# Kernel optimization log

Hardware: AMD Instinct MI355X
Metric: run time of the kernel (lower is better)

The kernel has to match this reference:

```python
import jax, jax.numpy as jnp
import numpy as np

N, IN_F, OUT_F, H = 8192, 256, 64, 4
NEG_SLOPE = 0.2


def setup_inputs() -> dict:
    key = jax.random.key(0)
    ks = jax.random.split(key, 8)
    inputs = jax.random.normal(ks[0], (N, IN_F), dtype=jnp.float32)
    # sparse-ish binary adjacency with self loops (sparse.softmax only sees nonzeros)
    adj = (jax.random.uniform(ks[1], (N, N)) < 0.05).astype(jnp.float32)
    idx = jnp.arange(N)
    adj = adj.at[idx, idx].set(1.0)
    stdv = 1.0 / np.sqrt(H * OUT_F)
    weight = jax.random.uniform(ks[2], (IN_F, H * OUT_F), minval=-stdv, maxval=stdv, dtype=jnp.float32)
    bias = jax.random.uniform(ks[3], (1, H * OUT_F), minval=-stdv, maxval=stdv, dtype=jnp.float32)
    # weight_u/v: stdv = 1/sqrt(size(-1)=1) = 1
    weight_u = jax.random.uniform(ks[4], (H, OUT_F, 1), minval=-1.0, maxval=1.0, dtype=jnp.float32)
    weight_v = jax.random.uniform(ks[5], (H, OUT_F, 1), minval=-1.0, maxval=1.0, dtype=jnp.float32)
    stdp = 1.0 / np.sqrt(IN_F)
    proj_w = jax.random.uniform(ks[6], (H * OUT_F, IN_F), minval=-stdp, maxval=stdp, dtype=jnp.float32)
    proj_b = jax.random.uniform(ks[7], (H * OUT_F,), minval=-stdp, maxval=stdp, dtype=jnp.float32)
    return {"inputs": inputs, "adj_mat": adj, "weight": weight, "weight_u": weight_u,
            "weight_v": weight_v, "bias": bias, "proj_w": proj_w, "proj_b": proj_b}


def reference(inputs, adj_mat, weight, weight_u, weight_v, bias, proj_w, proj_b):
    n = inputs.shape[0]
    support = (inputs @ weight).reshape(n, H, OUT_F).transpose(1, 0, 2)  # [H,N,O]
    f1 = jnp.einsum('hno,ho->hn', support, weight_u[..., 0])  # [H,N]
    f2 = jnp.einsum('hno,ho->hn', support, weight_v[..., 0])  # [H,N]
    logits = f1[:, None, :] + f2[:, :, None]                  # [H,N,N]
    w = jax.nn.leaky_relu(logits, NEG_SLOPE)
    masked = w * adj_mat                                      # adj broadcast over heads
    mask = adj_mat != 0.0
    # sparse.softmax over dim 2: softmax restricted to nonzero (edge) positions
    neg = jnp.where(mask, masked, -jnp.inf)
    m = jnp.max(neg, axis=2, keepdims=True)
    m = jnp.where(jnp.isfinite(m), m, 0.0)
    e = jnp.where(mask, jnp.exp(neg - m), 0.0)
    denom = jnp.sum(e, axis=2, keepdims=True)
    attn = e / jnp.where(denom > 0, denom, 1.0)               # [H,N,N]
    out = jnp.einsum('hnm,hmo->hno', attn, support)           # [H,N,O]
    out = out.transpose(1, 0, 2).reshape(n, H * OUT_F)
    out = out + bias
    out = out + inputs @ proj_w.T + proj_b
    return out
```

## Files before the change

### kernel.cpp

```cpp
#include <hip/hip_runtime.h>
#include <hip/hip_bf16.h>

#define N_NODES 8192
#define IN_FEAT 256
#define OUT_F   64
#define NHEAD   4
#define HF      256
#define NEG     0.2f

typedef unsigned short u16;
typedef unsigned char  u8;
typedef unsigned int   u32;
typedef unsigned long long u64;
typedef _Float16 h2    __attribute__((ext_vector_type(2)));
typedef _Float16 half8 __attribute__((ext_vector_type(8)));
typedef __attribute__((ext_vector_type(4))) float f32x4;

__global__ __launch_bounds__(256) void k_wpack(const float* __restrict__ W,
                                               const float* __restrict__ PW,
                                               _Float16* __restrict__ W16B) {
    const int i = blockIdx.x * 256 + threadIdx.x;
    const int ks = i >> 11;
    const int T  = (i >> 6) & 31;
    const int lane = i & 63;
    const int q  = lane >> 4, cc = lane & 15;
    const int n  = T * 16 + cc;
    const int k0 = ks * 32 + q * 8;
    union { _Float16 hh[8]; half8 v8; } o;
    #pragma unroll
    for (int e = 0; e < 8; ++e) {
        const int k = k0 + e;
        const float s = (n < 256) ? W[k * 256 + n]
                                  : PW[(size_t)(n - 256) * 256 + k];
        o.hh[e] = (_Float16)s;
    }
    *(half8*)(W16B + (size_t)i * 8) = o.v8;
}

#define GROWS 16
__global__ __launch_bounds__(256) void k_gemm(
    const float* __restrict__ inp,
    const _Float16* __restrict__ W16B,
    const float* __restrict__ U,
    const float* __restrict__ V,
    const float* __restrict__ Bias,
    const float* __restrict__ PB,
    _Float16* __restrict__ suppB,
    float* __restrict__ f1,
    float* __restrict__ f2,
    float* __restrict__ outp,
    float* __restrict__ anum,
    float* __restrict__ aden)
{
    __shared__ __align__(16) _Float16 xl[GROWS][264];
    const int n0  = blockIdx.x * GROWS;
    const int tid = threadIdx.x;
    const int wv  = tid >> 6, lane = tid & 63;
    const int col = lane & 15, quad = lane >> 4;

    {
        const int r = tid >> 4, seg = tid & 15;
        const float* src = inp + (size_t)(n0 + r) * 256 + seg * 16;
        const float4 v0 = *(const float4*)(src);
        const float4 v1 = *(const float4*)(src + 4);
        const float4 v2 = *(const float4*)(src + 8);
        const float4 v3 = *(const float4*)(src + 12);
        union { _Float16 hh[8]; half8 v; } c0, c1;
        c0.hh[0] = (_Float16)v0.x; c0.hh[1] = (_Float16)v0.y;
        c0.hh[2] = (_Float16)v0.z; c0.hh[3] = (_Float16)v0.w;
        c0.hh[4] = (_Float16)v1.x; c0.hh[5] = (_Float16)v1.y;
        c0.hh[6] = (_Float16)v1.z; c0.hh[7] = (_Float16)v1.w;
        c1.hh[0] = (_Float16)v2.x; c1.hh[1] = (_Float16)v2.y;
        c1.hh[2] = (_Float16)v2.z; c1.hh[3] = (_Float16)v2.w;
        c1.hh[4] = (_Float16)v3.x; c1.hh[5] = (_Float16)v3.y;
        c1.hh[6] = (_Float16)v3.z; c1.hh[7] = (_Float16)v3.w;
        *(half8*)&xl[r][seg * 16]     = c0.v;
        *(half8*)&xl[r][seg * 16 + 8] = c1.v;
    }
    __syncthreads();

    f32x4 acc[8];
    #pragma unroll
    for (int t = 0; t < 8; ++t) acc[t] = (f32x4){0.f, 0.f, 0.f, 0.f};

    const int qo = quad * 8;
    #pragma unroll
    for (int ks = 0; ks < 8; ++ks) {
        const half8 af = *(const half8*)&xl[col][ks * 32 + qo];
        const _Float16* bb = W16B + ((size_t)(ks * 32 + wv * 8) * 64 + lane) * 8;
        #pragma unroll
        for (int t = 0; t < 8; ++t) {
            const half8 bw = *(const half8*)(bb + (size_t)t * 512);
            acc[t] = __builtin_amdgcn_mfma_f32_16x16x32_f16(af, bw, acc[t], 0, 0, 0);
        }
    }

    if (wv < 2) {
        const int jbg  = n0 >> 5;
        const int nlo  = n0 & 31;
        const int jq   = nlo + quad * 4;
        const int e0   = jq & 7;
        const int wrow = (jq >> 3) << 4;
        #pragma unroll
        for (int t = 0; t < 8; ++t) {
            const int cg = wv * 128 + t * 16 + col;
            const int h  = cg >> 6;
            const int tp = (cg >> 4) & 3;
            union { _Float16 hh[4]; u64 q; } pk;
            #pragma unroll
            for (int reg = 0; reg < 4; ++reg) pk.hh[reg] = (_Float16)acc[t][reg];
            const size_t word = ((size_t)(h * 256 + jbg) * 4 + tp) * 64 + wrow + col;
            *(u64*)(suppB + word * 8 + e0) = pk.q;
        }
        float s1a[4] = {0,0,0,0}, s2a[4] = {0,0,0,0};
        float s1b[4] = {0,0,0,0}, s2b[4] = {0,0,0,0};
        #pragma unroll
        for (int t = 0; t < 8; ++t) {
            const int cg = wv * 128 + t * 16 + col;
            const float uu = U[cg], vv = V[cg];
            #pragma unroll
            for (int reg = 0; reg < 4; ++reg) {
                if (t < 4) { s1a[reg] += acc[t][reg] * uu; s2a[reg] += acc[t][reg] * vv; }
                else       { s1b[reg] += acc[t][reg] * uu; s2b[reg] += acc[t][reg] * vv; }
            }
        }
        #pragma unroll
        for (int m = 1; m < 16; m <<= 1) {
            #pragma unroll
            for (int reg = 0; reg < 4; ++reg) {
                s1a[reg] += __shfl_xor(s1a[reg], m);
                s2a[reg] += __shfl_xor(s2a[reg], m);
                s1b[reg] += __shfl_xor(s1b[reg], m);
                s2b[reg] += __shfl_xor(s2b[reg], m);
            }
        }
        if (col == 0) {
            const int hA = wv * 2, hB = wv * 2 + 1;
            #pragma unroll
            for (int reg = 0; reg < 4; ++reg) {
                const int n = n0 + quad * 4 + reg;
                f1[hA * N_NODES + n] = s1a[reg];
                f2[hA * N_NODES + n] = s2a[reg];
                f1[hB * N_NODES + n] = s1b[reg];
                f2[hB * N_NODES + n] = s2b[reg];
            }
        }
    } else {
        #pragma unroll
        for (int t = 0; t < 8; ++t) {
            const int cg = (wv - 2) * 128 + t * 16 + col;
            const float bb2 = Bias[cg] + PB[cg];
            #pragma unroll
            for (int reg = 0; reg < 4; ++reg) {
                const int irow = quad * 4 + reg;
                outp[(size_t)(n0 + irow) * HF + cg] = acc[t][reg] + bb2;
            }
        }
    }

    {
        const float4 z = {0.f, 0.f, 0.f, 0.f};
        float4* an = (float4*)(anum + (size_t)(n0 + (tid >> 4)) * HF + (tid & 15) * 16);
        an[0] = z; an[1] = z; an[2] = z; an[3] = z;
        if (tid < 64)
            aden[(size_t)(tid >> 4) * N_NODES + n0 + (tid & 15)] = 0.f;
    }
}

__global__ __launch_bounds__(256) void k_prep(const float* __restrict__ f1,
                                              float* __restrict__ f1max,
                                              _Float16* __restrict__ EA16,
                                              _Float16* __restrict__ EB16) {
    __shared__ float red[256];
    const int h = blockIdx.x;
    float m = -1e30f;
    for (int j = threadIdx.x; j < N_NODES; j += 256)
        m = fmaxf(m, f1[h * N_NODES + j]);
    red[threadIdx.x] = m;
    __syncthreads();
    for (int s = 128; s > 0; s >>= 1) {
        if (threadIdx.x < s) red[threadIdx.x] = fmaxf(red[threadIdx.x], red[threadIdx.x + s]);
        __syncthreads();
    }
    const float fm = red[0];
    if (threadIdx.x == 0) f1max[h] = fm;
    for (int j = threadIdx.x; j < N_NODES; j += 256) {
        const float d = f1[h * N_NODES + j] - fm;
        EA16[(size_t)h * N_NODES + j] = (_Float16)__expf(d);
        EB16[(size_t)h * N_NODES + j] = (_Float16)__expf(NEG * d);
    }
}

#define TI 64
#define NSUB 4
#define JSPLIT_G 8
#define JW (N_NODES / JSPLIT_G)
#define ABW 132

__global__ __launch_bounds__(256, 4) void k_attn_mfma(
    const float* __restrict__ adj,
    const _Float16* __restrict__ suppB,
    const _Float16* __restrict__ EA16,
    const _Float16* __restrict__ EB16,
    const float* __restrict__ f2,
    const float* __restrict__ f1max,
    float* __restrict__ anum,
    float* __restrict__ aden)
{
    __shared__ __align__(4) u8 abyte[TI][ABW];

    const int itile = blockIdx.x >> 3;
    const int jwin  = blockIdx.x & 7;
    const int i0    = itile * TI;
    const int J0    = jwin * JW;
    const int wv    = threadIdx.x >> 6;
    const int lane  = threadIdx.x & 63;
    const int col   = lane & 15;
    const int quad  = lane >> 4;

    #pragma unroll
    for (int pass = 0; pass < 8; ++pass) {
        const int r = (wv << 4) + pass * 2 + (lane >> 5);
        const int w = lane & 31;
        const float* ar = adj + (size_t)(i0 + r) * N_NODES + J0 + w * 32;
        unsigned wrd = 0;
        #pragma unroll
        for (int p = 0; p < 8; ++p) {
            const float4 a = *(const float4*)(ar + p * 4);
            const unsigned nib =
                (unsigned)(a.x != 0.f)        | ((unsigned)(a.y != 0.f) << 1) |
                ((unsigned)(a.z != 0.f) << 2) | ((unsigned)(a.w != 0.f) << 3);
            wrd |= nib << (p * 4);
        }
        *(unsigned*)&abyte[r][w * 4] = wrd;
    }
    __syncthreads();

    const int h = wv;
    const float fm = f1max[h];
    h2 caH[NSUB], cbH[NSUB];
    float ls[NSUB];
    #pragma unroll
    for (int s = 0; s < NSUB; ++s) {
        const float f2i = f2[(size_t)h * N_NODES + i0 + s * 16 + col];
        const float g  = fm + f2i;
        const float mi = fmaxf(g, NEG * g);
        const _Float16 ca = (_Float16)__expf(g - mi);
        const _Float16 cb = (_Float16)__expf(NEG * g - mi);
        caH[s][0] = ca; caH[s][1] = ca;
        cbH[s][0] = cb; cbH[s][1] = cb;
        ls[s] = 0.f;
    }
    const h2 ones = {(_Float16)1.0f, (_Float16)1.0f};

    const _Float16* gea = EA16 + (size_t)h * N_NODES + J0;
    const _Float16* geb = EB16 + (size_t)h * N_NODES + J0;
    const _Float16* sb  = suppB + (size_t)h * 524288
                        + (size_t)(J0 >> 5) * 2048 + lane * 8;

    f32x4 acc[NSUB][4];
    #pragma unroll
    for (int s = 0; s < NSUB; ++s)
        #pragma unroll
        for (int t = 0; t < 4; ++t)
            acc[s][t] = (f32x4){0.f, 0.f, 0.f, 0.f};

    const int qo = quad << 3;

    #pragma unroll 2
    for (int jb = 0; jb < JW; jb += 32) {
        const int jl = jb + qo;
        const _Float16* fp = sb + (size_t)(jb >> 5) * 2048;
        const half8 bv0 = *(const half8*)(fp);
        const half8 bv1 = *(const half8*)(fp + 512);
        const half8 bv2 = *(const half8*)(fp + 1024);
        const half8 bv3 = *(const half8*)(fp + 1536);

        union { half8 v; h2 pr[4]; } ea, eb;
        ea.v = *(const half8*)(gea + jl);
        eb.v = *(const half8*)(geb + jl);
        const int wo = (jb >> 3) + quad;

        #pragma unroll
        for (int s = 0; s < NSUB; ++s) {
            const unsigned gw = abyte[col + s * 16][wo];
            union { half8 v; unsigned w[4]; h2 pr[4]; } af;
            #pragma unroll
            for (int p = 0; p < 4; ++p) {
                const h2 pa = ea.pr[p] * caH[s];
                const h2 pb = eb.pr[p] * cbH[s];
                const h2 x  = __builtin_elementwise_max(pa, pb);
                const unsigned mlo = (unsigned)((int)(gw << (31 - 2 * p)) >> 31) & 0x0000FFFFu;
                const unsigned mhi = (unsigned)((int)(gw << (30 - 2 * p)) >> 31) & 0xFFFF0000u;
                union { h2 hh; unsigned u; } xu;
                xu.hh = x;
                xu.u &= (mlo | mhi);
                af.w[p] = xu.u;
                ls[s] = __builtin_amdgcn_fdot2(xu.hh, ones, ls[s], false);
            }
            acc[s][0] = __builtin_amdgcn_mfma_f32_16x16x32_f16(af.v, bv0, acc[s][0], 0, 0, 0);
            acc[s][1] = __builtin_amdgcn_mfma_f32_16x16x32_f16(af.v, bv1, acc[s][1], 0, 0, 0);
            acc[s][2] = __builtin_amdgcn_mfma_f32_16x16x32_f16(af.v, bv2, acc[s][2], 0, 0, 0);
            acc[s][3] = __builtin_amdgcn_mfma_f32_16x16x32_f16(af.v, bv3, acc[s][3], 0, 0, 0);
        }
    }

    #pragma unroll
    for (int s = 0; s < NSUB; ++s) {
        ls[s] += __shfl_xor(ls[s], 16);
        ls[s] += __shfl_xor(ls[s], 32);
    }
    if (quad == 0) {
        #pragma unroll
        for (int s = 0; s < NSUB; ++s)
            unsafeAtomicAdd(aden + (size_t)h * N_NODES + i0 + s * 16 + col, ls[s]);
    }

    #pragma unroll
    for (int s = 0; s < NSUB; ++s) {
        #pragma unroll
        for (int reg = 0; reg < 4; ++reg) {
            const int irow = (quad << 2) + reg;
            float* ap = anum + (size_t)(i0 + s * 16 + irow) * HF + (h << 6) + col;
            #pragma unroll
            for (int t = 0; t < 4; ++t)
                unsafeAtomicAdd(ap + (t << 4), acc[s][t][reg]);
        }
    }
}

__global__ __launch_bounds__(256) void k_fin(const float* __restrict__ anum,
                                             const float* __restrict__ aden,
                                             float* __restrict__ out) {
    const int c = threadIdx.x;
    const int h = c >> 6;
    #pragma unroll
    for (int rr = 0; rr < 4; ++rr) {
        const int n = blockIdx.x * 4 + rr;
        out[(size_t)n * HF + c] += anum[(size_t)n * HF + c]
                                 / aden[(size_t)h * N_NODES + n];
    }
}

extern "C" void kernel_launch(void* const* d_in, const int* in_sizes, int n_in,
                              void* d_out, int out_size, void* d_ws, size_t ws_size,
                              hipStream_t stream) {
    const float* inp  = (const float*)d_in[0];
    const float* adj  = (const float*)d_in[1];
    const float* W    = (const float*)d_in[2];
    const float* U    = (const float*)d_in[3];
    const float* V    = (const float*)d_in[4];
    const float* Bias = (const float*)d_in[5];
    const float* PW   = (const float*)d_in[6];
    const float* PB   = (const float*)d_in[7];
    float* out = (float*)d_out;

    char* ws = (char*)d_ws;
    _Float16* suppB = (_Float16*)(ws);
    float* f1    = (float*)(ws + (4u << 20));
    float* f2    = (float*)(ws + (4u << 20) + (128u << 10));
    float* f1mx  = (float*)(ws + (4u << 20) + (256u << 10));
    _Float16* EA16 = (_Float16*)(ws + (4u << 20) + (576u << 10));
    _Float16* EB16 = (_Float16*)(ws + (4u << 20) + (704u << 10));
    float* aden  = (float*)(ws + (4u << 20) + (832u << 10));
    _Float16* W16B = (_Float16*)(ws + (20u << 20));
    float* anum  = (float*)(ws + (24u << 20));

    k_wpack<<<  64, 256, 0, stream>>>(W, PW, W16B);
    k_gemm <<< 512, 256, 0, stream>>>(inp, W16B, U, V, Bias, PB,
                                      suppB, f1, f2, out, anum, aden);
    k_prep <<<NHEAD, 256, 0, stream>>>(f1, f1mx, EA16, EB16);
    k_attn_mfma<<<(N_NODES / TI) * JSPLIT_G, 256, 0, stream>>>(
        adj, suppB, EA16, EB16, f2, f1mx, anum, aden);
    k_fin  <<<N_NODES / 4, 256, 0, stream>>>(anum, aden, out);
}
```

Baseline: 454.2 us.

## Pack adjacency bitmask in GEMM kernel and split attention J into 16 windows

The fp32 adjacency-to-bitmask conversion moves out of the attention kernel into the tail of the projection GEMM kernel, which writes a global packed bitmask. The attention kernel then loads only the compact bitmask for its tile. The J dimension is split 16 ways instead of 8, and the occupancy hint rises to 5 blocks per CU. Each of the 256 MB adjacency reads now happens in the GEMM kernel, which may serialise badly with only 512 blocks. Doubling the J split also doubles the atomic or partial accumulation traffic into anum and aden.

```diff
diff --git a/kernel.cpp b/kernel.cpp
--- a/kernel.cpp
+++ b/kernel.cpp
@@ -40,6 +40,7 @@
 #define GROWS 16
 __global__ __launch_bounds__(256) void k_gemm(
     const float* __restrict__ inp,
+    const float* __restrict__ adj,
     const _Float16* __restrict__ W16B,
     const float* __restrict__ U,
     const float* __restrict__ V,
@@ -49,6 +50,7 @@
     float* __restrict__ f1,
     float* __restrict__ f2,
     float* __restrict__ outp,
+    u32*   __restrict__ gb32,
     float* __restrict__ anum,
     float* __restrict__ aden)
 {
@@ -165,6 +167,27 @@
         if (tid < 64)
             aden[(size_t)(tid >> 4) * N_NODES + n0 + (tid & 15)] = 0.f;
     }
+
+    #pragma unroll 1
+    for (int rr = 0; rr < 4; ++rr) {
+        const int r = n0 + (wv << 2) + rr;
+        const float* ar = adj + (size_t)r * N_NODES;
+        u32* gr = gb32 + (size_t)r * 256;
+        #pragma unroll
+        for (int pi = 0; pi < 4; ++pi) {
+            const float* as = ar + pi * 2048 + lane * 32;
+            u32 wrd = 0;
+            #pragma unroll
+            for (int p = 0; p < 8; ++p) {
+                const float4 a = *(const float4*)(as + p * 4);
+                const u32 nib =
+                    (u32)(a.x != 0.f)        | ((u32)(a.y != 0.f) << 1) |
+                    ((u32)(a.z != 0.f) << 2) | ((u32)(a.w != 0.f) << 3);
+                wrd |= nib << (p * 4);
+            }
+            gr[pi * 64 + lane] = wrd;
+        }
+    }
 }
 
 __global__ __launch_bounds__(256) void k_prep(const float* __restrict__ f1,
@@ -193,12 +216,11 @@
 
 #define TI 64
 #define NSUB 4
-#define JSPLIT_G 8
+#define JSPLIT_G 16
 #define JW (N_NODES / JSPLIT_G)
-#define ABW 132
-
-__global__ __launch_bounds__(256, 4) void k_attn_mfma(
-    const float* __restrict__ adj,
+
+__global__ __launch_bounds__(256, 5) void k_attn_mfma(
+    const u32* __restrict__ gb32,
     const _Float16* __restrict__ suppB,
     const _Float16* __restrict__ EA16,
     const _Float16* __restrict__ EB16,
@@ -207,32 +229,24 @@
     float* __restrict__ anum,
     float* __restrict__ aden)
 {
-    __shared__ __align__(4) u8 abyte[TI][ABW];
-
-    const int itile = blockIdx.x >> 3;
-    const int jwin  = blockIdx.x & 7;
+    __shared__ __align__(16) u8 abyte[TI][80];
+
+    const int itile = blockIdx.x >> 4;
+    const int jwin  = blockIdx.x & 15;
     const int i0    = itile * TI;
     const int J0    = jwin * JW;
-    const int wv    = threadIdx.x >> 6;
-    const int lane  = threadIdx.x & 63;
+    const int tid   = threadIdx.x;
+    const int wv    = tid >> 6;
+    const int lane  = tid & 63;
     const int col   = lane & 15;
     const int quad  = lane >> 4;
 
-    #pragma unroll
-    for (int pass = 0; pass < 8; ++pass) {
-        const int r = (wv << 4) + pass * 2 + (lane >> 5);
-        const int w = lane & 31;
-        const float* ar = adj + (size_t)(i0 + r) * N_NODES + J0 + w * 32;
-        unsigned wrd = 0;
-        #pragma unroll
-        for (int p = 0; p < 8; ++p) {
-            const float4 a = *(const float4*)(ar + p * 4);
-            const unsigned nib =
-                (unsigned)(a.x != 0.f)        | ((unsigned)(a.y != 0.f) << 1) |
-                ((unsigned)(a.z != 0.f) << 2) | ((unsigned)(a.w != 0.f) << 3);
-            wrd |= nib << (p * 4);
-        }
-        *(unsigned*)&abyte[r][w * 4] = wrd;
+    {
+        const int r  = tid >> 2;
+        const int wi = tid & 3;
+        const uint4 fw = *(const uint4*)(gb32 + (size_t)(i0 + r) * 256
+                                         + (J0 >> 5) + wi * 4);
+        *(uint4*)&abyte[r][wi * 16] = fw;
     }
     __syncthreads();
 
@@ -363,14 +377,15 @@
     _Float16* EA16 = (_Float16*)(ws + (4u << 20) + (576u << 10));
     _Float16* EB16 = (_Float16*)(ws + (4u << 20) + (704u << 10));
     float* aden  = (float*)(ws + (4u << 20) + (832u << 10));
+    u32*   gb32  = (u32*)(ws + (8u << 20));
     _Float16* W16B = (_Float16*)(ws + (20u << 20));
     float* anum  = (float*)(ws + (24u << 20));
 
     k_wpack<<<  64, 256, 0, stream>>>(W, PW, W16B);
-    k_gemm <<< 512, 256, 0, stream>>>(inp, W16B, U, V, Bias, PB,
-                                      suppB, f1, f2, out, anum, aden);
+    k_gemm <<< 512, 256, 0, stream>>>(inp, adj, W16B, U, V, Bias, PB,
+                                      suppB, f1, f2, out, gb32, anum, aden);
     k_prep <<<NHEAD, 256, 0, stream>>>(f1, f1mx, EA16, EB16);
     k_attn_mfma<<<(N_NODES / TI) * JSPLIT_G, 256, 0, stream>>>(
-        adj, suppB, EA16, EB16, f2, f1mx, anum, aden);
+        gb32, suppB, EA16, EB16, f2, f1mx, anum, aden);
     k_fin  <<<N_NODES / 4, 256, 0, stream>>>(anum, aden, out);
 }
```

Measured after the change: 680.1 us. +49.8%, slower.
